# Performance work log

Measured on AMD Instinct MI355X. Metric: run time of the kernel, lower is better.

The kernel has to match this reference:

```python
import jax, jax.numpy as jnp
import numpy as np
from jax import lax

START_IDX = 0
STOP_IDX = 1


def _forward_alg(feats_lbt, mask_lb, transitions):
    # feats_lbt: [L, B, T], mask_lb: [L, B], transitions[i, j] = score(j -> i)
    L, B, T = feats_lbt.shape
    init = jnp.full((B, T), -10000.0, dtype=feats_lbt.dtype).at[:, START_IDX].set(0.0)

    def step(fv, xs):
        feat, m = xs  # feat: [B, T], m: [B]
        # scores[b, next, prev] = fv[b, prev] + transitions[next, prev] + feat[b, next]
        scores = fv[:, None, :] + transitions[None, :, :] + feat[:, :, None]
        alphas = jax.nn.logsumexp(scores, axis=-1)  # [B, T]
        fv = jnp.where(m[:, None] > 0, alphas, fv)
        return fv, None

    fv, _ = lax.scan(step, init, (feats_lbt, mask_lb))
    terminal = fv + transitions[STOP_IDX][None, :]
    return jax.nn.logsumexp(terminal, axis=-1)  # [B]


def _score_sentence(feats_lbt, tags_bl, mask_lb, transitions):
    L, B, T = feats_lbt.shape
    start_col = jnp.full((B, 1), START_IDX, dtype=tags_bl.dtype)
    tags_ext = jnp.concatenate([start_col, tags_bl], axis=-1)  # [B, L+1]
    # transition scores along the gold path: [B, L]
    trans = transitions[tags_ext[:, 1:], tags_ext[:, :-1]]
    # emission scores: feats is [L, B, T] -> gather per-position gold tag
    emit = jnp.take_along_axis(
        feats_lbt, tags_bl.T[:, :, None], axis=-1
    )[:, :, 0]  # [L, B]
    step_scores = (trans.T + emit) * (mask_lb > 0)  # [L, B]
    score = step_scores.sum(axis=0)  # [B]
    lengths = mask_lb.sum(axis=0).astype(jnp.int32)  # [B]
    last_tag = tags_ext[jnp.arange(B), lengths]
    score = score + transitions[STOP_IDX, last_tag]
    return score


def setup_inputs() -> dict:
    key = jax.random.key(0)
    k1, k2, k3 = jax.random.split(key, 3)
    B, L, T = 256, 2048, 32
    efeats = jax.random.normal(k1, (B, L, T), dtype=jnp.float32)
    mask = jnp.ones((B, L), dtype=jnp.float32)
    tgt = jax.random.randint(k2, (B, L), 0, T, dtype=jnp.int32)
    transitions = jax.random.normal(k3, (T, T), dtype=jnp.float32)
    return {"efeats": efeats, "mask": mask, "tgt": tgt, "transitions": transitions}


def reference(efeats, mask, tgt, transitions):
    B, L = mask.shape
    mask_lb = mask.T  # [L, B]
    feats_lbt = jnp.transpose(efeats, (1, 0, 2))  # [L, B, T]
    forward_score = _forward_alg(feats_lbt, mask_lb, transitions)
    gold_score = _score_sentence(feats_lbt, tgt, mask_lb, transitions)
    loss = (forward_score - gold_score).sum() / B
    return loss
```

## Files before the change

kernel.cpp:

```cpp
#include <hip/hip_runtime.h>

#define B_SZ 256
#define L_SZ 2048
#define T_SZ 32
#define START_IDX 0
#define STOP_IDX 1

#define CLEN 64
#define NPAIR 32
#define NSLOT 8
#define NMAT_SEQ 4
#define NBLK_TOT (B_SZ * NMAT_SEQ)

#define FB_NCH 16
#define FB_CLEN 128

#define SCALE_LN 4.1588830833596718565f

typedef __attribute__((ext_vector_type(8))) short bf16x8;
typedef __attribute__((ext_vector_type(4))) float f32x4;
typedef __attribute__((ext_vector_type(2))) float f32x2;

__device__ __forceinline__ unsigned fau(float f){ union{float f; unsigned u;} v; v.f=f; return v.u; }
__device__ __forceinline__ float uaf(unsigned u){ union{unsigned u; float f;} v; v.u=u; return v.f; }
__device__ __forceinline__ int pack_trunc(float lo, float hi){
  return (int)__builtin_amdgcn_perm(fau(hi), fau(lo), 0x07060302u);
}
__device__ __forceinline__ bf16x8 frag_of(const int* p){
  union{ int i[4]; bf16x8 v; } u;
  u.i[0]=p[0]; u.i[1]=p[1]; u.i[2]=p[2]; u.i[3]=p[3];
  return u.v;
}

__device__ __forceinline__ void mfma4(bf16x8 A0, bf16x8 A1, bf16x8 B0, bf16x8 B1,
                                      f32x4& c00, f32x4& c01, f32x4& c10, f32x4& c11)
{
  const f32x4 z = {0.f,0.f,0.f,0.f};
  asm("s_nop 1\n\t"
      "v_mfma_f32_16x16x32_bf16 %0, %4, %5, %8\n\t"
      "v_mfma_f32_16x16x32_bf16 %1, %4, %6, %8\n\t"
      "v_mfma_f32_16x16x32_bf16 %2, %7, %5, %8\n\t"
      "v_mfma_f32_16x16x32_bf16 %3, %7, %6, %8\n\t"
      "s_nop 7\n\t"
      "s_nop 7"
      : "=&v"(c00), "=&v"(c01), "=&v"(c10), "=&v"(c11)
      : "v"(A0), "v"(B0), "v"(B1), "v"(A1), "v"(z));
}

__device__ __forceinline__ void mfma8(bf16x8 A0, bf16x8 A1,
                                      bf16x8 Ba0, bf16x8 Ba1, bf16x8 Bb0, bf16x8 Bb1,
                                      f32x4& a00, f32x4& a01, f32x4& a10, f32x4& a11,
                                      f32x4& b00, f32x4& b01, f32x4& b10, f32x4& b11)
{
  const f32x4 z = {0.f,0.f,0.f,0.f};
  asm("s_nop 1\n\t"
      "v_mfma_f32_16x16x32_bf16 %0, %8, %10, %14\n\t"
      "v_mfma_f32_16x16x32_bf16 %1, %8, %11, %14\n\t"
      "v_mfma_f32_16x16x32_bf16 %2, %9, %10, %14\n\t"
      "v_mfma_f32_16x16x32_bf16 %3, %9, %11, %14\n\t"
      "v_mfma_f32_16x16x32_bf16 %4, %8, %12, %14\n\t"
      "v_mfma_f32_16x16x32_bf16 %5, %8, %13, %14\n\t"
      "v_mfma_f32_16x16x32_bf16 %6, %9, %12, %14\n\t"
      "v_mfma_f32_16x16x32_bf16 %7, %9, %13, %14\n\t"
      "s_nop 7\n\t"
      "s_nop 7"
      : "=&v"(a00), "=&v"(a01), "=&v"(a10), "=&v"(a11),
        "=&v"(b00), "=&v"(b01), "=&v"(b10), "=&v"(b11)
      : "v"(A0), "v"(A1), "v"(Ba0), "v"(Ba1), "v"(Bb0), "v"(Bb1), "v"(z));
}

__global__ void zero_kernel(float* out){ if(threadIdx.x==0) out[0]=0.f; }

__device__ __forceinline__ int mat_prod(const unsigned short* L, const unsigned short* Rt,
                                        unsigned short* dst, bool writeT, int lane)
{
  const int g = lane >> 4, c16 = lane & 15;
  const int ko = 8*g;
  bf16x8 A0 = *(const bf16x8*)(L  + (c16*T_SZ      + ko));
  bf16x8 A1 = *(const bf16x8*)(L  + ((16+c16)*T_SZ + ko));
  bf16x8 B0 = *(const bf16x8*)(Rt + (c16*T_SZ      + ko));
  bf16x8 B1 = *(const bf16x8*)(Rt + ((16+c16)*T_SZ + ko));
  f32x4 q00,q01,q10,q11;
  mfma4(A0, A1, B0, B1, q00, q01, q10, q11);

  unsigned mb = (unsigned)__builtin_amdgcn_readfirstlane((int)fau(q00[0]));
  int e = (int)((mb>>23)&255u) - 127;
  float r = uaf((unsigned)(127-e)<<23);
  #pragma unroll
  for (int i=0;i<4;++i){ q00[i]*=r; q01[i]*=r; q10[i]*=r; q11[i]*=r; }

  if (!writeT){
    #pragma unroll
    for (int reg=0; reg<4; ++reg){
      int x0 = 4*g + reg, x1 = 16 + 4*g + reg;
      dst[x0*T_SZ + c16]      = (unsigned short)(fau(q00[reg])>>16);
      dst[x0*T_SZ + 16 + c16] = (unsigned short)(fau(q01[reg])>>16);
      dst[x1*T_SZ + c16]      = (unsigned short)(fau(q10[reg])>>16);
      dst[x1*T_SZ + 16 + c16] = (unsigned short)(fau(q11[reg])>>16);
    }
  } else {
    #pragma unroll
    for (int rp=0; rp<2; ++rp){
      int xb0 = 4*g + 2*rp, xb1 = 16 + 4*g + 2*rp;
      *(int*)&dst[c16*T_SZ + xb0]        = pack_trunc(q00[2*rp], q00[2*rp+1]);
      *(int*)&dst[(16+c16)*T_SZ + xb0]   = pack_trunc(q01[2*rp], q01[2*rp+1]);
      *(int*)&dst[c16*T_SZ + xb1]        = pack_trunc(q10[2*rp], q10[2*rp+1]);
      *(int*)&dst[(16+c16)*T_SZ + xb1]   = pack_trunc(q11[2*rp], q11[2*rp+1]);
    }
  }
  return e;
}

__global__ __launch_bounds__(256, 4) void crf_chunk_kernel(
    const float* __restrict__ efeats, const float* __restrict__ mask,
    const int* __restrict__ tgt, const float* __restrict__ trans,
    unsigned short* __restrict__ wsM, int* __restrict__ wsE,
    float* __restrict__ wsG, float* __restrict__ wsL,
    float* __restrict__ out)
{
  __shared__ float s_trans[T_SZ*T_SZ];
  __shared__ float s_d[4][256];
  __shared__ unsigned short s_tree[NSLOT][T_SZ*T_SZ];
  __shared__ int   s_et[NSLOT];
  __shared__ float s_gd[4], s_ml[4];

  const int tid  = threadIdx.x;
  const int w    = tid >> 6;
  const int lane = tid & 63;
  const int g    = lane >> 4;
  const int c16  = lane & 15;

  const int b  = blockIdx.x >> 2;
  const int q  = blockIdx.x & 3;
  const int l0A = q*(NSLOT*CLEN) + (2*w)*CLEN;
  const int l0B = l0A + CLEN;

  if (blockIdx.x == 0 && tid == 0) out[0] = 0.f;

  #pragma unroll
  for (int i=0;i<4;++i) s_trans[tid + i*256] = trans[tid + i*256];
  __syncthreads();

  bf16x8 A0f, A1f;
  {
    int a0i[4], a1i[4];
    #pragma unroll
    for (int I=0; I<2; ++I){
      int row = 8*(c16>>2) + 4*I + (c16&3);
      float e[8];
      #pragma unroll
      for (int j=0;j<8;++j) e[j] = __expf(s_trans[row*T_SZ + 8*g + j]);
      int* dst = I ? a1i : a0i;
      #pragma unroll
      for (int p=0;p<4;++p) dst[p] = pack_trunc(e[2*p], e[2*p+1]);
    }
    A0f = frag_of(a0i); A1f = frag_of(a1i);
  }

  int b0a[4], b1a[4], b0b[4], b1b[4];
  #pragma unroll
  for (int p=0;p<4;++p){
    int s0 = 8*g + 2*p, s1 = s0+1;
    unsigned lo = (s0==c16)?0x3f80u:0u, hi = (s1==c16)?0x3f80u:0u;
    b0a[p] = (int)(lo | (hi<<16));  b0b[p] = b0a[p];
    lo = (s0==16+c16)?0x3f80u:0u; hi = (s1==16+c16)?0x3f80u:0u;
    b1a[p] = (int)(lo | (hi<<16));  b1b[p] = b1a[p];
  }

  const long fbase = ((long)b * L_SZ) * T_SZ;
  const int  mbA = b*L_SZ + l0A;
  const int  mbB = b*L_SZ + l0B;

  float mA = mask[mbA + lane];
  float mB = mask[mbB + lane];
  int   tA = tgt [mbA + lane];
  int   tB = tgt [mbB + lane];
  int   tpA = (l0A + lane == 0) ? START_IDX : tgt[mbA + lane - 1];
  int   tpB = tgt[mbB + lane - 1];

  float emA = efeats[fbase + (long)(l0A+lane)*T_SZ + tA];
  float emB = efeats[fbase + (long)(l0B+lane)*T_SZ + tB];
  float gl = ((mA > 0.f) ? (s_trans[tA*T_SZ + tpA] + emA) : 0.f)
           + ((mB > 0.f) ? (s_trans[tB*T_SZ + tpB] + emB) : 0.f);
  float ml = mA + mB;
  #pragma unroll
  for (int off=32; off>0; off>>=1){ gl += __shfl_xor(gl, off, 64); ml += __shfl_xor(ml, off, 64); }

  unsigned long long mba = __ballot(mA > 0.f);
  unsigned long long mbb = __ballot(mB > 0.f);

  const float* fptA = efeats + fbase + (long)l0A*T_SZ;
  const float* fptB = efeats + fbase + (long)l0B*T_SZ;
  float* s_dwA = &s_d[w][0];
  float* s_dwB = &s_d[w][128];

  float fqa[4], fqb[4];
  #pragma unroll
  for (int i=1; i<=4; ++i){ fqa[i&3] = fptA[i*64 + lane]; fqb[i&3] = fptB[i*64 + lane]; }
  s_dwA[lane] = __expf(fptA[lane] - SCALE_LN);
  s_dwB[lane] = __expf(fptB[lane] - SCALE_LN);

  if ((mba & mbb) == ~0ull){
    #pragma unroll 2
    for (int p=0; p<NPAIR; ++p){
      s_dwA[((p+1)&1)*64 + lane] = __expf(fqa[(p+1)&3] - SCALE_LN);
      s_dwB[((p+1)&1)*64 + lane] = __expf(fqb[(p+1)&3] - SCALE_LN);
      int np = p+5; np = (np > NPAIR-1) ? (NPAIR-1) : np;
      fqa[(p+1)&3] = fptA[np*64 + lane];
      fqb[(p+1)&3] = fptB[np*64 + lane];
      const float* dbA = &s_dwA[(p&1)*64];
      const float* dbB = &s_dwB[(p&1)*64];
      #pragma unroll
      for (int h=0; h<2; ++h){
        f32x4 cA00,cA01,cA10,cA11, cB00,cB01,cB10,cB11;
        mfma8(A0f, A1f, frag_of(b0a), frag_of(b1a), frag_of(b0b), frag_of(b1b),
              cA00,cA01,cA10,cA11, cB00,cB01,cB10,cB11);

        const float4* dvA = (const float4*)(dbA + h*32);
        const float4* dvB = (const float4*)(dbB + h*32);
        float4 dlA = dvA[2*g], dhA = dvA[2*g+1];
        float4 dlB = dvB[2*g], dhB = dvB[2*g+1];

        {
          f32x2 q0={cA00[0],cA00[1]}; q0 *= (f32x2){dlA.x,dlA.y};
          f32x2 q1={cA00[2],cA00[3]}; q1 *= (f32x2){dlA.z,dlA.w};
          f32x2 q2={cA01[0],cA01[1]}; q2 *= (f32x2){dlA.x,dlA.y};
          f32x2 q3={cA01[2],cA01[3]}; q3 *= (f32x2){dlA.z,dlA.w};
          f32x2 q4={cA10[0],cA10[1]}; q4 *= (f32x2){dhA.x,dhA.y};
          f32x2 q5={cA10[2],cA10[3]}; q5 *= (f32x2){dhA.z,dhA.w};
          f32x2 q6={cA11[0],cA11[1]}; q6 *= (f32x2){dhA.x,dhA.y};
          f32x2 q7={cA11[2],cA11[3]}; q7 *= (f32x2){dhA.z,dhA.w};
          b0a[0]=pack_trunc(q0[0],q0[1]); b0a[1]=pack_trunc(q1[0],q1[1]);
          b0a[2]=pack_trunc(q4[0],q4[1]); b0a[3]=pack_trunc(q5[0],q5[1]);
          b1a[0]=pack_trunc(q2[0],q2[1]); b1a[1]=pack_trunc(q3[0],q3[1]);
          b1a[2]=pack_trunc(q6[0],q6[1]); b1a[3]=pack_trunc(q7[0],q7[1]);
        }
        {
          f32x2 q0={cB00[0],cB00[1]}; q0 *= (f32x2){dlB.x,dlB.y};
          f32x2 q1={cB00[2],cB00[3]}; q1 *= (f32x2){dlB.z,dlB.w};
          f32x2 q2={cB01[0],cB01[1]}; q2 *= (f32x2){dlB.x,dlB.y};
          f32x2 q3={cB01[2],cB01[3]}; q3 *= (f32x2){dlB.z,dlB.w};
          f32x2 q4={cB10[0],cB10[1]}; q4 *= (f32x2){dhB.x,dhB.y};
          f32x2 q5={cB10[2],cB10[3]}; q5 *= (f32x2){dhB.z,dhB.w};
          f32x2 q6={cB11[0],cB11[1]}; q6 *= (f32x2){dhB.x,dhB.y};
          f32x2 q7={cB11[2],cB11[3]}; q7 *= (f32x2){dhB.z,dhB.w};
          b0b[0]=pack_trunc(q0[0],q0[1]); b0b[1]=pack_trunc(q1[0],q1[1]);
          b0b[2]=pack_trunc(q4[0],q4[1]); b0b[3]=pack_trunc(q5[0],q5[1]);
          b1b[0]=pack_trunc(q2[0],q2[1]); b1b[1]=pack_trunc(q3[0],q3[1]);
          b1b[2]=pack_trunc(q6[0],q6[1]); b1b[3]=pack_trunc(q7[0],q7[1]);
        }
      }
    }
  } else {
    for (int p=0; p<NPAIR; ++p){
      s_dwA[((p+1)&1)*64 + lane] = __expf(fqa[(p+1)&3] - SCALE_LN);
      s_dwB[((p+1)&1)*64 + lane] = __expf(fqb[(p+1)&3] - SCALE_LN);
      int np = p+5; if (np > NPAIR-1) np = NPAIR-1;
      fqa[(p+1)&3] = fptA[np*64 + lane];
      fqb[(p+1)&3] = fptB[np*64 + lane];
      const float* dbA = &s_dwA[(p&1)*64];
      const float* dbB = &s_dwB[(p&1)*64];
      #pragma unroll
      for (int h=0; h<2; ++h){
        int t = 2*p + h;
        f32x4 cA00,cA01,cA10,cA11, cB00,cB01,cB10,cB11;
        mfma8(A0f, A1f, frag_of(b0a), frag_of(b1a), frag_of(b0b), frag_of(b1b),
              cA00,cA01,cA10,cA11, cB00,cB01,cB10,cB11);

        if ((mba >> t) & 1ull){
          const float4* dvA = (const float4*)(dbA + h*32);
          float4 dl = dvA[2*g], dh2 = dvA[2*g+1];
          float f0=dl.x, f1=dl.y, f2=dl.z, f3=dl.w;
          float f4=dh2.x, f5=dh2.y, f6=dh2.z, f7=dh2.w;
          cA00[0]*=f0; cA00[1]*=f1; cA00[2]*=f2; cA00[3]*=f3;
          cA01[0]*=f0; cA01[1]*=f1; cA01[2]*=f2; cA01[3]*=f3;
          cA10[0]*=f4; cA10[1]*=f5; cA10[2]*=f6; cA10[3]*=f7;
          cA11[0]*=f4; cA11[1]*=f5; cA11[2]*=f6; cA11[3]*=f7;
          b0a[0]=pack_trunc(cA00[0],cA00[1]); b0a[1]=pack_trunc(cA00[2],cA00[3]);
          b0a[2]=pack_trunc(cA10[0],cA10[1]); b0a[3]=pack_trunc(cA10[2],cA10[3]);
          b1a[0]=pack_trunc(cA01[0],cA01[1]); b1a[1]=pack_trunc(cA01[2],cA01[3]);
          b1a[2]=pack_trunc(cA11[0],cA11[1]); b1a[3]=pack_trunc(cA11[2],cA11[3]);
        }
        if ((mbb >> t) & 1ull){
          const float4* dvB = (const float4*)(dbB + h*32);
          float4 dl = dvB[2*g], dh2 = dvB[2*g+1];
          float f0=dl.x, f1=dl.y, f2=dl.z, f3=dl.w;
          float f4=dh2.x, f5=dh2.y, f6=dh2.z, f7=dh2.w;
          cB00[0]*=f0; cB00[1]*=f1; cB00[2]*=f2; cB00[3]*=f3;
          cB01[0]*=f0; cB01[1]*=f1; cB01[2]*=f2; cB01[3]*=f3;
          cB10[0]*=f4; cB10[1]*=f5; cB10[2]*=f6; cB10[3]*=f7;
          cB11[0]*=f4; cB11[1]*=f5; cB11[2]*=f6; cB11[3]*=f7;
          b0b[0]=pack_trunc(cB00[0],cB00[1]); b0b[1]=pack_trunc(cB00[2],cB00[3]);
          b0b[2]=pack_trunc(cB10[0],cB10[1]); b0b[3]=pack_trunc(cB10[2],cB10[3]);
          b1b[0]=pack_trunc(cB01[0],cB01[1]); b1b[1]=pack_trunc(cB01[2],cB01[3]);
          b1b[2]=pack_trunc(cB11[0],cB11[1]); b1b[3]=pack_trunc(cB11[2],cB11[3]);
        }
      }
    }
  }

  {
    unsigned short* S = &s_tree[2*w][0];
    #pragma unroll
    for (int p=0;p<4;++p){
      int s = 8*g + 2*p;
      *(int*)&S[c16*T_SZ + s]      = b0a[p];
      *(int*)&S[(16+c16)*T_SZ + s] = b1a[p];
    }
    unsigned short* St = &s_tree[2*w+1][0];
    #pragma unroll
    for (int p=0;p<4;++p){
      int s = 8*g + 2*p;
      St[s*T_SZ + c16]          = (unsigned short)(b0b[p] & 0xffff);
      St[(s+1)*T_SZ + c16]      = (unsigned short)(((unsigned)b0b[p])>>16);
      St[s*T_SZ + 16 + c16]     = (unsigned short)(b1b[p] & 0xffff);
      St[(s+1)*T_SZ + 16 + c16] = (unsigned short)(((unsigned)b1b[p])>>16);
    }
  }
  if (lane==0){
    s_et[2*w]   = 6 * __popcll(mba);
    s_et[2*w+1] = 6 * __popcll(mbb);
    s_gd[w] = gl; s_ml[w] = ml;
  }
  __syncthreads();

  {
    int e = mat_prod(&s_tree[2*w][0], &s_tree[2*w+1][0], &s_tree[2*w][0], (w&1)!=0, lane);
    if (lane==0) s_et[2*w] = s_et[2*w] + s_et[2*w+1] + e;
  }
  __syncthreads();
  if (w < 2){
    int e = mat_prod(&s_tree[4*w][0], &s_tree[4*w+2][0], &s_tree[4*w][0], (w&1)!=0, lane);
    if (lane==0) s_et[4*w] = s_et[4*w] + s_et[4*w+2] + e;
  }
  __syncthreads();
  if (w == 0){
    int e = mat_prod(&s_tree[0][0], &s_tree[4][0], &s_tree[0][0], false, lane);
    if (lane==0) s_et[0] = s_et[0] + s_et[4] + e;
  }
  __syncthreads();

  const int bid = blockIdx.x;
  ((int*)(wsM + (long)bid*(T_SZ*T_SZ)))[tid]       = ((const int*)&s_tree[0][0])[tid];
  ((int*)(wsM + (long)bid*(T_SZ*T_SZ)))[tid + 256] = ((const int*)&s_tree[0][0])[tid + 256];
  if (tid == 0){
    wsE[bid] = s_et[0];
    float gs=0.f, ls=0.f;
    #pragma unroll
    for (int i=0;i<4;++i){ gs += s_gd[i]; ls += s_ml[i]; }
    wsG[bid] = gs; wsL[bid] = ls;
  }
}

__global__ __launch_bounds__(64) void crf_combine_kernel(
    const unsigned short* __restrict__ wsM, const int* __restrict__ wsE,
    const float* __restrict__ wsG, const float* __restrict__ wsL,
    const int* __restrict__ tgt, const float* __restrict__ trans,
    float* __restrict__ out)
{
  __shared__ unsigned short sM[NMAT_SEQ*T_SZ*T_SZ];
  __shared__ float s_v[T_SZ];

  const int tid = threadIdx.x;
  const int b   = blockIdx.x;

  const uint4* src = (const uint4*)(wsM + (long)b*NMAT_SEQ*T_SZ*T_SZ);
  #pragma unroll
  for (int i=0;i<NMAT_SEQ*2;++i) ((uint4*)sM)[tid + i*64] = src[tid + i*64];
  __syncthreads();

  const int s = tid & 31;
  float v = (s==START_IDX)?1.f:0.f;
  int E = 0;
  #pragma unroll
  for (int j=0; j<NMAT_SEQ; ++j){
    if (tid < 32) s_v[s] = v;
    __syncthreads();
    const unsigned short* M = &sM[j*T_SZ*T_SZ];
    float u = 0.f;
    #pragma unroll 8
    for (int x=0; x<T_SZ; ++x){
      float mv = uaf(((unsigned)M[x*T_SZ + s])<<16);
      u = fmaf(mv, s_v[x], u);
    }
    unsigned ub = (unsigned)__builtin_amdgcn_readfirstlane((int)fau(u));
    int eu = (int)((ub>>23)&255u)-127;
    E += wsE[b*NMAT_SEQ + j] + eu;
    v = u * uaf((unsigned)(127-eu)<<23);
    __syncthreads();
  }
  float term = v * __expf(trans[STOP_IDX*T_SZ + s]);
  #pragma unroll
  for (int off=16; off>0; off>>=1) term += __shfl_xor(term, off, 32);
  float fwd = (float)E * 0.69314718055994530942f + __logf(term);

  if (tid == 0){
    float gp = 0.f, lp = 0.f;
    #pragma unroll
    for (int j=0;j<NMAT_SEQ;++j){ gp += wsG[b*NMAT_SEQ+j]; lp += wsL[b*NMAT_SEQ+j]; }
    int len = (int)lp;
    int last_tag = (len==0)? START_IDX : tgt[b*L_SZ + len-1];
    float goldT = gp + trans[STOP_IDX*T_SZ + last_tag];
    atomicAdd(out, (fwd - goldT) * (1.0f/B_SZ));
  }
}

__global__ __launch_bounds__(1024) void crf_loss_kernel(
    const float* __restrict__ efeats, const float* __restrict__ mask,
    const int* __restrict__ tgt, const float* __restrict__ trans,
    float* __restrict__ out)
{
  __shared__ float s_trans[T_SZ*T_SZ];
  __shared__ float s_d[FB_NCH][T_SZ];
  __shared__ unsigned short s_M[FB_NCH][T_SZ*T_SZ];
  __shared__ int   s_es[FB_NCH];
  __shared__ float s_gd[FB_NCH];
  __shared__ float s_mlv[FB_NCH];

  const int tid  = threadIdx.x;
  const int b    = blockIdx.x;
  const int w    = tid >> 6;
  const int lane = tid & 63;
  const int g    = lane >> 4;
  const int c16  = lane & 15;
  const int i32  = lane & 31;

  s_trans[tid] = trans[tid];
  __syncthreads();

  int a0[4], a1[4];
  #pragma unroll
  for (int I=0; I<2; ++I){
    int row = 8*(c16>>2) + 4*I + (c16&3);
    float e[8];
    #pragma unroll
    for (int j=0;j<8;++j) e[j] = __expf(s_trans[row*T_SZ + 8*g + j]);
    int* dst = I ? a1 : a0;
    #pragma unroll
    for (int p=0;p<4;++p) dst[p] = pack_trunc(e[2*p], e[2*p+1]);
  }

  int b0[4], b1[4];
  #pragma unroll
  for (int p=0;p<4;++p){
    int s0 = 8*g + 2*p, s1 = s0+1;
    unsigned lo = (s0==c16)?0x3f80u:0u, hi = (s1==c16)?0x3f80u:0u;
    b0[p] = (int)(lo | (hi<<16));
    lo = (s0==16+c16)?0x3f80u:0u; hi = (s1==16+c16)?0x3f80u:0u;
    b1[p] = (int)(lo | (hi<<16));
  }

  const int l0 = w * FB_CLEN;
  const long fbase = ((long)b * L_SZ) * T_SZ;

  float fqv[4];
  #pragma unroll
  for (int i=0;i<4;++i) fqv[i] = efeats[fbase + (long)(l0+i)*T_SZ + i32];

  int   tA = tgt [b*L_SZ + l0 + lane];
  int   tB = tgt [b*L_SZ + l0 + 64 + lane];
  float mA = mask[b*L_SZ + l0 + lane];
  float mB = mask[b*L_SZ + l0 + 64 + lane];
  int prev = (l0==0) ? START_IDX : tgt[b*L_SZ + l0 - 1];

  int esum = 0;
  float gold = 0.f, mlen = 0.f;
  const f32x4 zf = {0.f,0.f,0.f,0.f};

  #pragma unroll 4
  for (int t=0; t<FB_CLEN; ++t){
    float fcur = fqv[t&3];
    int lpf = l0 + t + 4; lpf = (lpf < L_SZ) ? lpf : (L_SZ-1);
    fqv[t&3] = efeats[fbase + (long)lpf*T_SZ + i32];

    float mk  = uaf((unsigned)__builtin_amdgcn_readlane((int)fau((t<64)?mA:mB), t&63));
    int   cur = __builtin_amdgcn_readlane((t<64)?tA:tB, t&63);
    mlen += mk;

    if (mk > 0.f){
      if (lane < 32) s_d[w][lane] = __expf(fcur);

      f32x4 c00 = __builtin_amdgcn_mfma_f32_16x16x32_bf16(frag_of(a0), frag_of(b0), zf, 0,0,0);
      f32x4 c01 = __builtin_amdgcn_mfma_f32_16x16x32_bf16(frag_of(a0), frag_of(b1), zf, 0,0,0);
      f32x4 c10 = __builtin_amdgcn_mfma_f32_16x16x32_bf16(frag_of(a1), frag_of(b0), zf, 0,0,0);
      f32x4 c11 = __builtin_amdgcn_mfma_f32_16x16x32_bf16(frag_of(a1), frag_of(b1), zf, 0,0,0);

      const float4* dv = (const float4*)(&s_d[w][0]);
      float4 dl = dv[2*g], dh = dv[2*g+1];
      float f0=dl.x, f1=dl.y, f2=dl.z, f3=dl.w;
      float f4=dh.x, f5=dh.y, f6=dh.z, f7=dh.w;

      float m00 = c00[0]*f0;
      unsigned mb = (unsigned)__builtin_amdgcn_readfirstlane((int)fau(m00));
      int e = (int)((mb>>23)&255u) - 127;
      esum += e;
      float r = uaf((unsigned)(127-e)<<23);
      f0*=r; f1*=r; f2*=r; f3*=r; f4*=r; f5*=r; f6*=r; f7*=r;

      c00[0]*=f0; c00[1]*=f1; c00[2]*=f2; c00[3]*=f3;
      c01[0]*=f0; c01[1]*=f1; c01[2]*=f2; c01[3]*=f3;
      c10[0]*=f4; c10[1]*=f5; c10[2]*=f6; c10[3]*=f7;
      c11[0]*=f4; c11[1]*=f5; c11[2]*=f6; c11[3]*=f7;

      b0[0]=pack_trunc(c00[0],c00[1]); b0[1]=pack_trunc(c00[2],c00[3]);
      b0[2]=pack_trunc(c10[0],c10[1]); b0[3]=pack_trunc(c10[2],c10[3]);
      b1[0]=pack_trunc(c01[0],c01[1]); b1[1]=pack_trunc(c01[2],c01[3]);
      b1[2]=pack_trunc(c11[0],c11[1]); b1[3]=pack_trunc(c11[2],c11[3]);

      float tp   = s_trans[cur*T_SZ + prev];
      float emit = uaf((unsigned)__builtin_amdgcn_readlane((int)fau(fcur), cur));
      gold += tp + emit;
    }
    prev = cur;
  }

  #pragma unroll
  for (int p=0;p<4;++p){
    int s = 8*g + 2*p;
    *(int*)((char*)(&s_M[w][0]) + (((long)(c16   )*T_SZ + s) * 2)) = b0[p];
    *(int*)((char*)(&s_M[w][0]) + (((long)(16+c16)*T_SZ + s) * 2)) = b1[p];
  }
  if (lane==0){ s_es[w]=esum; s_gd[w]=gold; s_mlv[w]=mlen; }
  __syncthreads();

  if (w==0){
    int s = i32;
    float v = (s==START_IDX)?1.f:0.f;
    int E = 0;
    for (int c=0;c<FB_NCH;++c){
      float u=0.f;
      #pragma unroll 8
      for (int k=0;k<T_SZ;++k){
        float mv = uaf(((unsigned)s_M[c][k*T_SZ + s])<<16);
        float vk = uaf((unsigned)__builtin_amdgcn_readlane((int)fau(v), k));
        u = fmaf(mv, vk, u);
      }
      unsigned ub = (unsigned)__builtin_amdgcn_readfirstlane((int)fau(u));
      int eu = (int)((ub>>23)&255u)-127;
      E += s_es[c] + eu;
      v = u * uaf((unsigned)(127-eu)<<23);
    }
    float term = v * __expf(s_trans[STOP_IDX*T_SZ + s]);
    #pragma unroll
    for (int off=16; off>0; off>>=1) term += __shfl_xor(term, off, 32);
    float fwd = (float)E * 0.69314718055994530942f + __logf(term);

    float gp = (s<FB_NCH)? s_gd[s] : 0.f;
    float lp = (s<FB_NCH)? s_mlv[s] : 0.f;
    #pragma unroll
    for (int off=16; off>0; off>>=1){ gp += __shfl_xor(gp, off, 32); lp += __shfl_xor(lp, off, 32); }
    int len = (int)lp;
    int last_tag = (len==0)? START_IDX : tgt[b*L_SZ + (len-1)];
    float goldT = gp + s_trans[STOP_IDX*T_SZ + last_tag];
    if (tid==0) atomicAdd(out, (fwd - goldT) * (1.0f/B_SZ));
  }
}

extern "C" void kernel_launch(void* const* d_in, const int* in_sizes, int n_in,
                              void* d_out, int out_size, void* d_ws, size_t ws_size,
                              hipStream_t stream)
{
  const float* efeats = (const float*)d_in[0];
  const float* mask   = (const float*)d_in[1];
  const int*   tgt    = (const int*)d_in[2];
  const float* trans  = (const float*)d_in[3];
  float* out = (float*)d_out;

  const size_t needM = (size_t)NBLK_TOT * T_SZ * T_SZ * 2;
  const size_t need  = needM + (size_t)NBLK_TOT * 12;

  if (ws_size >= need){
    unsigned short* wsM = (unsigned short*)d_ws;
    char* p = (char*)d_ws + needM;
    int*   wsE = (int*)p;
    float* wsG = (float*)(p + (size_t)NBLK_TOT*4);
    float* wsL = (float*)(p + (size_t)NBLK_TOT*8);
    crf_chunk_kernel<<<dim3(NBLK_TOT), dim3(256), 0, stream>>>(
        efeats, mask, tgt, trans, wsM, wsE, wsG, wsL, out);
    crf_combine_kernel<<<dim3(B_SZ), dim3(64), 0, stream>>>(
        wsM, wsE, wsG, wsL, tgt, trans, out);
  } else {
    zero_kernel<<<dim3(1), dim3(64), 0, stream>>>(out);
    crf_loss_kernel<<<dim3(B_SZ), dim3(1024), 0, stream>>>(efeats, mask, tgt, trans, out);
  }
}
```

Before: 141.1 us.

## Software-pipeline the two chains so MFMA of one overlaps pack of the other

The fast path of the chunked matrix-chain loop is restructured so the MFMA for chain B is issued while chain A's results are scaled and packed, and the other way round. This replaces the fused 8-MFMA block followed by long s_nop padding with interleaved 4-MFMA groups. Scale factors are preloaded into registers from shared memory one step ahead, and sched_barriers fix the instruction order. The aim is to hide MFMA latency and the LDS reads behind VALU work, at the cost of more live registers and reliance on hand-ordered hazard timing, since the volatile mfma4v has no trailing nops.

```diff
diff --git a/kernel.cpp b/kernel.cpp
--- a/kernel.cpp
+++ b/kernel.cpp
@@ -31,6 +31,21 @@
   u.i[0]=p[0]; u.i[1]=p[1]; u.i[2]=p[2]; u.i[3]=p[3];
   return u.v;
 }
+
+#define PACKQ(c00,c01,c10,c11, dl,dh2, o0,o1) do{ \
+  f32x2 q0={c00[0],c00[1]}; q0 *= (f32x2){dl.x,dl.y};   \
+  f32x2 q1={c00[2],c00[3]}; q1 *= (f32x2){dl.z,dl.w};   \
+  f32x2 q2={c01[0],c01[1]}; q2 *= (f32x2){dl.x,dl.y};   \
+  f32x2 q3={c01[2],c01[3]}; q3 *= (f32x2){dl.z,dl.w};   \
+  f32x2 q4={c10[0],c10[1]}; q4 *= (f32x2){dh2.x,dh2.y}; \
+  f32x2 q5={c10[2],c10[3]}; q5 *= (f32x2){dh2.z,dh2.w}; \
+  f32x2 q6={c11[0],c11[1]}; q6 *= (f32x2){dh2.x,dh2.y}; \
+  f32x2 q7={c11[2],c11[3]}; q7 *= (f32x2){dh2.z,dh2.w}; \
+  o0[0]=pack_trunc(q0[0],q0[1]); o0[1]=pack_trunc(q1[0],q1[1]); \
+  o0[2]=pack_trunc(q4[0],q4[1]); o0[3]=pack_trunc(q5[0],q5[1]); \
+  o1[0]=pack_trunc(q2[0],q2[1]); o1[1]=pack_trunc(q3[0],q3[1]); \
+  o1[2]=pack_trunc(q6[0],q6[1]); o1[3]=pack_trunc(q7[0],q7[1]); \
+}while(0)
 
 __device__ __forceinline__ void mfma4(bf16x8 A0, bf16x8 A1, bf16x8 B0, bf16x8 B1,
                                       f32x4& c00, f32x4& c01, f32x4& c10, f32x4& c11)
@@ -43,6 +58,20 @@
       "v_mfma_f32_16x16x32_bf16 %3, %7, %6, %8\n\t"
       "s_nop 7\n\t"
       "s_nop 7"
+      : "=&v"(c00), "=&v"(c01), "=&v"(c10), "=&v"(c11)
+      : "v"(A0), "v"(B0), "v"(B1), "v"(A1), "v"(z));
+}
+
+__device__ __forceinline__ void mfma4v(bf16x8 A0, bf16x8 A1, bf16x8 B0, bf16x8 B1,
+                                       f32x4& c00, f32x4& c01, f32x4& c10, f32x4& c11)
+{
+  const f32x4 z = {0.f,0.f,0.f,0.f};
+  asm volatile(
+      "s_nop 1\n\t"
+      "v_mfma_f32_16x16x32_bf16 %0, %4, %5, %8\n\t"
+      "v_mfma_f32_16x16x32_bf16 %1, %4, %6, %8\n\t"
+      "v_mfma_f32_16x16x32_bf16 %2, %7, %5, %8\n\t"
+      "v_mfma_f32_16x16x32_bf16 %3, %7, %6, %8"
       : "=&v"(c00), "=&v"(c01), "=&v"(c10), "=&v"(c11)
       : "v"(A0), "v"(B0), "v"(B1), "v"(A1), "v"(z));
 }
@@ -129,6 +158,7 @@
   const int lane = tid & 63;
   const int g    = lane >> 4;
   const int c16  = lane & 15;
+  const int gq   = 2*g;
 
   const int b  = blockIdx.x >> 2;
   const int q  = blockIdx.x & 3;
@@ -201,55 +231,58 @@
   s_dwB[lane] = __expf(fptB[lane] - SCALE_LN);
 
   if ((mba & mbb) == ~0ull){
-    #pragma unroll 2
+    float4 dA0,dA1,dA2,dA3, dB0,dB1,dB2,dB3;
+    {
+      const float4* va = (const float4*)(s_dwA);
+      const float4* vb = (const float4*)(s_dwB);
+      dA0 = va[gq]; dA1 = va[gq+1]; dA2 = va[8+gq]; dA3 = va[8+gq+1];
+      dB0 = vb[gq]; dB1 = vb[gq+1]; dB2 = vb[8+gq]; dB3 = vb[8+gq+1];
+    }
+    f32x4 cA00,cA01,cA10,cA11, cB00,cB01,cB10,cB11;
+
+    mfma4(A0f, A1f, frag_of(b0a), frag_of(b1a), cA00,cA01,cA10,cA11);
+    __builtin_amdgcn_sched_barrier(0);
+
+    #pragma unroll 4
     for (int p=0; p<NPAIR; ++p){
-      s_dwA[((p+1)&1)*64 + lane] = __expf(fqa[(p+1)&3] - SCALE_LN);
-      s_dwB[((p+1)&1)*64 + lane] = __expf(fqb[(p+1)&3] - SCALE_LN);
+      const int nb = ((p+1)&1)*64;
       int np = p+5; np = (np > NPAIR-1) ? (NPAIR-1) : np;
+
+      mfma4v(A0f, A1f, frag_of(b0b), frag_of(b1b), cB00,cB01,cB10,cB11);
+      __builtin_amdgcn_sched_barrier(0);
+
+      PACKQ(cA00,cA01,cA10,cA11, dA0,dA1, b0a,b1a);
+      s_dwA[nb + lane] = __expf(fqa[(p+1)&3] - SCALE_LN);
       fqa[(p+1)&3] = fptA[np*64 + lane];
+      __builtin_amdgcn_sched_barrier(0);
+
+      mfma4v(A0f, A1f, frag_of(b0a), frag_of(b1a), cA00,cA01,cA10,cA11);
+      __builtin_amdgcn_sched_barrier(0);
+
+      PACKQ(cB00,cB01,cB10,cB11, dB0,dB1, b0b,b1b);
+      s_dwB[nb + lane] = __expf(fqb[(p+1)&3] - SCALE_LN);
       fqb[(p+1)&3] = fptB[np*64 + lane];
-      const float* dbA = &s_dwA[(p&1)*64];
-      const float* dbB = &s_dwB[(p&1)*64];
-      #pragma unroll
-      for (int h=0; h<2; ++h){
-        f32x4 cA00,cA01,cA10,cA11, cB00,cB01,cB10,cB11;
-        mfma8(A0f, A1f, frag_of(b0a), frag_of(b1a), frag_of(b0b), frag_of(b1b),
-              cA00,cA01,cA10,cA11, cB00,cB01,cB10,cB11);
-
-        const float4* dvA = (const float4*)(dbA + h*32);
-        const float4* dvB = (const float4*)(dbB + h*32);
-        float4 dlA = dvA[2*g], dhA = dvA[2*g+1];
-        float4 dlB = dvB[2*g], dhB = dvB[2*g+1];
-
-        {
-          f32x2 q0={cA00[0],cA00[1]}; q0 *= (f32x2){dlA.x,dlA.y};
-          f32x2 q1={cA00[2],cA00[3]}; q1 *= (f32x2){dlA.z,dlA.w};
-          f32x2 q2={cA01[0],cA01[1]}; q2 *= (f32x2){dlA.x,dlA.y};
-          f32x2 q3={cA01[2],cA01[3]}; q3 *= (f32x2){dlA.z,dlA.w};
-          f32x2 q4={cA10[0],cA10[1]}; q4 *= (f32x2){dhA.x,dhA.y};
-          f32x2 q5={cA10[2],cA10[3]}; q5 *= (f32x2){dhA.z,dhA.w};
-          f32x2 q6={cA11[0],cA11[1]}; q6 *= (f32x2){dhA.x,dhA.y};
-          f32x2 q7={cA11[2],cA11[3]}; q7 *= (f32x2){dhA.z,dhA.w};
-          b0a[0]=pack_trunc(q0[0],q0[1]); b0a[1]=pack_trunc(q1[0],q1[1]);
-          b0a[2]=pack_trunc(q4[0],q4[1]); b0a[3]=pack_trunc(q5[0],q5[1]);
-          b1a[0]=pack_trunc(q2[0],q2[1]); b1a[1]=pack_trunc(q3[0],q3[1]);
-          b1a[2]=pack_trunc(q6[0],q6[1]); b1a[3]=pack_trunc(q7[0],q7[1]);
-        }
-        {
-          f32x2 q0={cB00[0],cB00[1]}; q0 *= (f32x2){dlB.x,dlB.y};
-          f32x2 q1={cB00[2],cB00[3]}; q1 *= (f32x2){dlB.z,dlB.w};
-          f32x2 q2={cB01[0],cB01[1]}; q2 *= (f32x2){dlB.x,dlB.y};
-          f32x2 q3={cB01[2],cB01[3]}; q3 *= (f32x2){dlB.z,dlB.w};
-          f32x2 q4={cB10[0],cB10[1]}; q4 *= (f32x2){dhB.x,dhB.y};
-          f32x2 q5={cB10[2],cB10[3]}; q5 *= (f32x2){dhB.z,dhB.w};
-          f32x2 q6={cB11[0],cB11[1]}; q6 *= (f32x2){dhB.x,dhB.y};
-          f32x2 q7={cB11[2],cB11[3]}; q7 *= (f32x2){dhB.z,dhB.w};
-          b0b[0]=pack_trunc(q0[0],q0[1]); b0b[1]=pack_trunc(q1[0],q1[1]);
-          b0b[2]=pack_trunc(q4[0],q4[1]); b0b[3]=pack_trunc(q5[0],q5[1]);
-          b1b[0]=pack_trunc(q2[0],q2[1]); b1b[1]=pack_trunc(q3[0],q3[1]);
-          b1b[2]=pack_trunc(q6[0],q6[1]); b1b[3]=pack_trunc(q7[0],q7[1]);
-        }
+      __builtin_amdgcn_sched_barrier(0);
+
+      mfma4v(A0f, A1f, frag_of(b0b), frag_of(b1b), cB00,cB01,cB10,cB11);
+      __builtin_amdgcn_sched_barrier(0);
+
+      PACKQ(cA00,cA01,cA10,cA11, dA2,dA3, b0a,b1a);
+      {
+        const float4* va = (const float4*)(s_dwA + nb);
+        dA0 = va[gq]; dA1 = va[gq+1]; dA2 = va[8+gq]; dA3 = va[8+gq+1];
       }
+      __builtin_amdgcn_sched_barrier(0);
+
+      mfma4v(A0f, A1f, frag_of(b0a), frag_of(b1a), cA00,cA01,cA10,cA11);
+      __builtin_amdgcn_sched_barrier(0);
+
+      PACKQ(cB00,cB01,cB10,cB11, dB2,dB3, b0b,b1b);
+      {
+        const float4* vb = (const float4*)(s_dwB + nb);
+        dB0 = vb[gq]; dB1 = vb[gq+1]; dB2 = vb[8+gq]; dB3 = vb[8+gq+1];
+      }
+      __builtin_amdgcn_sched_barrier(0);
     }
   } else {
     for (int p=0; p<NPAIR; ++p){
```

After: 139.1 us. No clear change (-1.4%).
